# Kernel optimization log

Hardware: AMD Instinct MI355X
Metric: run time of the kernel (lower is better)

The kernel has to match this reference:

```python
import jax, jax.numpy as jnp
import numpy as np

N = 100000  # nodes
E = 1600000  # edges
N_IN, N_H = 256, 128


def _norms(edge_src, edge_dst):
    ones = jnp.ones((E,), dtype=jnp.float32)
    out_deg = jax.ops.segment_sum(ones, edge_src, num_segments=N)
    in_deg = jax.ops.segment_sum(ones, edge_dst, num_segments=N)
    # DGL clamps degrees to >= 1 for norm='both'
    norm_src = jnp.clip(out_deg, 1.0, None) ** -0.5  # [N]
    norm_dst = jnp.clip(in_deg, 1.0, None) ** -0.5   # [N]
    return norm_src, norm_dst


def _graph_conv(h, W, b, edge_src, edge_dst, norm_src, norm_dst):
    # symmetric norm: D_out^{-1/2} A D_in^{-1/2}; W applied pre-aggregation
    h = h * norm_src[:, None]          # [N, d_in]
    h = h @ W                          # [N, d_out]
    msg = h[edge_src]                  # [E, d_out] gather
    agg = jax.ops.segment_sum(msg, edge_dst, num_segments=N)  # scatter-add
    agg = agg * norm_dst[:, None]
    return jax.nn.relu(agg + b)


def setup_inputs() -> dict:
    key = jax.random.key(0)
    ks = jax.random.split(key, 7)
    feat = jax.random.normal(ks[0], (1, N, N_IN), dtype=jnp.float32)
    edge_src = jax.random.randint(ks[1], (E,), 0, N, dtype=jnp.int32)
    edge_dst = jax.random.randint(ks[2], (E,), 0, N, dtype=jnp.int32)
    # Glorot-uniform weights as in DGL GraphConv reset_parameters
    lim1 = (6.0 / (N_IN + N_H)) ** 0.5
    lim2 = (6.0 / (N_H + N_H)) ** 0.5
    W1 = jax.random.uniform(ks[3], (N_IN, N_H), jnp.float32, -lim1, lim1)
    b1 = jnp.zeros((N_H,), dtype=jnp.float32)
    W2 = jax.random.uniform(ks[4], (N_H, N_H), jnp.float32, -lim2, lim2)
    b2 = jnp.zeros((N_H,), dtype=jnp.float32)
    return {"feat": feat, "W1": W1, "b1": b1, "W2": W2, "b2": b2,
            "edge_src": edge_src, "edge_dst": edge_dst}


def reference(feat, W1, b1, W2, b2, edge_src, edge_dst):
    h = feat.squeeze(0)  # [N, n_in]
    norm_src, norm_dst = _norms(edge_src, edge_dst)
    h = _graph_conv(h, W1, b1, edge_src, edge_dst, norm_src, norm_dst)
    h = _graph_conv(h, W2, b2, edge_src, edge_dst, norm_src, norm_dst)
    return h
```

## Files before the change

### kernel.cpp

```cpp
#include <hip/hip_runtime.h>
#include <hip/hip_bf16.h>

#define N_NODES 100000
#define N_EDGES 1600000
#define NBUCK 391
#define NBLK 256
#define CHUNK (N_EDGES / NBLK)
#define MATP (NBUCK * NBLK)

typedef __bf16 bf16x8 __attribute__((ext_vector_type(8)));
typedef float f32x4 __attribute__((ext_vector_type(4)));
typedef unsigned short u16x8 __attribute__((ext_vector_type(8)));
typedef _Float16 f16x8 __attribute__((ext_vector_type(8)));

__device__ __forceinline__ unsigned short f32_to_bf16_rne(float x) {
    unsigned int u = __float_as_uint(x);
    unsigned int r = u + 0x7FFFu + ((u >> 16) & 1u);
    return (unsigned short)(r >> 16);
}
__device__ __forceinline__ float bf16_bits_to_f32(unsigned short h) {
    return __uint_as_float(((unsigned int)h) << 16);
}

__device__ __forceinline__ void wtsplit_elem(const float* __restrict__ W,
                                             unsigned short* __restrict__ WTh,
                                             unsigned short* __restrict__ WTl,
                                             int K, int i) {
    int col = i / K, k = i - col * K;
    float x = W[(size_t)k * 128 + col];
    unsigned short h = f32_to_bf16_rne(x);
    unsigned short l = f32_to_bf16_rne(x - bf16_bits_to_f32(h));
    WTh[i] = h;
    WTl[i] = l;
}

__global__ __launch_bounds__(256) void fused_setup(
    const int* __restrict__ esrc, const int* __restrict__ edst,
    int* __restrict__ cnt_mat,
    const float* __restrict__ W1, unsigned short* __restrict__ WT1h,
    unsigned short* __restrict__ WT1l,
    const float* __restrict__ W2, unsigned short* __restrict__ WT2h,
    unsigned short* __restrict__ WT2l)
{
    __shared__ int hd[NBUCK], hs[NBUCK];
    const int b = blockIdx.x, t = threadIdx.x;
    if (b < NBLK) {
        for (int i = t; i < NBUCK; i += 256) { hd[i] = 0; hs[i] = 0; }
        __syncthreads();
        const int e1 = (b + 1) * CHUNK;
        for (int e = b * CHUNK + t; e < e1; e += 256) {
            atomicAdd(&hd[edst[e] >> 8], 1);
            atomicAdd(&hs[esrc[e] >> 8], 1);
        }
        __syncthreads();
        for (int i = t; i < NBUCK; i += 256) {
            cnt_mat[i * NBLK + b] = hd[i];
            cnt_mat[MATP + i * NBLK + b] = hs[i];
        }
    } else {
        int i = (b - NBLK) * 256 + t;
        if (i < 128 * 256) {
            wtsplit_elem(W1, WT1h, WT1l, 256, i);
        } else {
            int j = i - 128 * 256;
            wtsplit_elem(W2, WT2h, WT2l, 128, j);
        }
    }
}

__global__ __launch_bounds__(1024) void scan_blocks(const int* __restrict__ counts,
                                                    int* __restrict__ out,
                                                    int* __restrict__ partials, int n) {
    __shared__ int tmp[1024];
    int i = blockIdx.x * 1024 + threadIdx.x;
    int v = (i < n) ? counts[i] : 0;
    tmp[threadIdx.x] = v;
    __syncthreads();
    for (int off = 1; off < 1024; off <<= 1) {
        int t = (threadIdx.x >= (unsigned)off) ? tmp[threadIdx.x - off] : 0;
        __syncthreads();
        tmp[threadIdx.x] += t;
        __syncthreads();
    }
    if (i < n) out[i] = tmp[threadIdx.x] - v;
    if (threadIdx.x == 1023) partials[blockIdx.x] = tmp[1023];
}

__global__ void scan_partials(int* __restrict__ partials, int nb) {
    if (threadIdx.x == 0 && blockIdx.x == 0) {
        int s = 0;
        for (int b = 0; b < nb; ++b) { int t = partials[b]; partials[b] = s; s += t; }
    }
}

__device__ __forceinline__ int sm_at(const int* __restrict__ scan_mat,
                                     const int* __restrict__ partials, int i) {
    return scan_mat[i] + partials[i >> 10];
}

__global__ __launch_bounds__(256) void bucket_scatter(const int* __restrict__ esrc,
                                                      const int* __restrict__ edst,
                                                      const int* __restrict__ scan_mat,
                                                      const int* __restrict__ partials,
                                                      unsigned int* __restrict__ tmp) {
    __shared__ int cd[NBUCK], cs[NBUCK];
    const int b = blockIdx.x, t = threadIdx.x;
    for (int i = t; i < NBUCK; i += 256) {
        cd[i] = sm_at(scan_mat, partials, i * NBLK + b);
        cs[i] = sm_at(scan_mat, partials, MATP + i * NBLK + b);
    }
    __syncthreads();
    const int e1 = (b + 1) * CHUNK;
    for (int e = b * CHUNK + t; e < e1; e += 256) {
        int s = esrc[e], d = edst[e];
        int pd = atomicAdd(&cd[d >> 8], 1);
        tmp[pd] = ((unsigned int)(d & 255) << 17) | (unsigned int)s;
        int ps = atomicAdd(&cs[s >> 8], 1);
        tmp[ps] = (unsigned int)s;
    }
}

__global__ __launch_bounds__(256) void finalize_fused(
    const unsigned int* __restrict__ tmp,
    const int* __restrict__ scan_mat,
    const int* __restrict__ partials,
    int* __restrict__ rowptr,
    int* __restrict__ csr_src,
    float* __restrict__ ndst,
    float* __restrict__ nsrc)
{
    __shared__ int hist[256];
    __shared__ int scn[256];
    __shared__ int cur[256];
    const int bb = blockIdx.x, t = threadIdx.x;
    if (bb < NBUCK) {
        const int b = bb;
        const int beg = sm_at(scan_mat, partials, b * 256);
        const int end = sm_at(scan_mat, partials, (b + 1) * 256);
        hist[t] = 0;
        __syncthreads();
        for (int j = beg + t; j < end; j += 256)
            atomicAdd(&hist[tmp[j] >> 17], 1);
        __syncthreads();
        int v = hist[t];
        scn[t] = v;
        __syncthreads();
        for (int off = 1; off < 256; off <<= 1) {
            int u = (t >= off) ? scn[t - off] : 0;
            __syncthreads();
            scn[t] += u;
            __syncthreads();
        }
        int excl = scn[t] - v;
        int node = b * 256 + t;
        if (node <= N_NODES) rowptr[node] = beg + excl;
        if (node < N_NODES) ndst[node] = rsqrtf(fmaxf((float)v, 1.0f));
        cur[t] = beg + excl;
        __syncthreads();
        for (int j = beg + t; j < end; j += 256) {
            unsigned int x = tmp[j];
            int pos = atomicAdd(&cur[x >> 17], 1);
            csr_src[pos] = (int)(x & 0x1FFFFu);
        }
    } else {
        const int b = bb - NBUCK;
        const int beg = sm_at(scan_mat, partials, MATP + b * 256);
        const int end = (b < NBUCK - 1) ? sm_at(scan_mat, partials, MATP + (b + 1) * 256)
                                        : 2 * N_EDGES;
        hist[t] = 0;
        __syncthreads();
        for (int j = beg + t; j < end; j += 256)
            atomicAdd(&hist[tmp[j] & 255u], 1);
        __syncthreads();
        int node = b * 256 + t;
        if (node < N_NODES) nsrc[node] = rsqrtf(fmaxf((float)hist[t], 1.0f));
    }
}

template<int K, typename AT>
__global__ __launch_bounds__(256) void gemm_mfma(
    const AT* __restrict__ A,
    const unsigned short* __restrict__ WTh,
    const unsigned short* __restrict__ WTl,
    const float* __restrict__ rowscale,
    _Float16* __restrict__ C16,
    int M)
{
    constexpr int ASTR = 520;
    constexpr int BSTR = 1032;
    __shared__ unsigned short Ah[4 * ASTR];
    __shared__ unsigned short Al[4 * ASTR];
    __shared__ unsigned short Bh[4 * BSTR];
    __shared__ unsigned short Bl[4 * BSTR];

    const int tid = threadIdx.x;
    const int bm = blockIdx.x * 64;
    const int lane = tid & 63;
    const int wid = tid >> 6;
    const int wm = wid >> 1;
    const int wn = wid & 1;
    const int lr = lane & 15;
    const int lg = lane >> 4;

    const int st_ar = tid >> 2;
    const int st_s8 = tid & 3;
    const int a_row_g = bm + st_ar;

    f32x4 acc[2][4];
    #pragma unroll
    for (int i = 0; i < 2; ++i)
        #pragma unroll
        for (int j = 0; j < 4; ++j)
            acc[i][j] = (f32x4){0.f, 0.f, 0.f, 0.f};

    float avreg[8];
    u16x8 bvh[2], bvl[2];

    auto load_tile = [&](int k0) {
        if (a_row_g < M) {
            const AT* ap = &A[(size_t)a_row_g * K + k0 + st_s8 * 8];
            if constexpr (sizeof(AT) == 4) {
                float4 v0 = *reinterpret_cast<const float4*>(ap);
                float4 v1 = *reinterpret_cast<const float4*>(ap + 4);
                avreg[0] = v0.x; avreg[1] = v0.y; avreg[2] = v0.z; avreg[3] = v0.w;
                avreg[4] = v1.x; avreg[5] = v1.y; avreg[6] = v1.z; avreg[7] = v1.w;
            } else {
                f16x8 v = *reinterpret_cast<const f16x8*>(ap);
                #pragma unroll
                for (int j = 0; j < 8; ++j) avreg[j] = (float)v[j];
            }
        } else {
            #pragma unroll
            for (int j = 0; j < 8; ++j) avreg[j] = 0.f;
        }
        #pragma unroll
        for (int i = 0; i < 2; ++i) {
            int lin = tid + i * 256;
            int col = lin >> 2;
            int s8  = lin & 3;
            const size_t g = (size_t)col * K + k0 + s8 * 8;
            bvh[i] = *reinterpret_cast<const u16x8*>(&WTh[g]);
            bvl[i] = *reinterpret_cast<const u16x8*>(&WTl[g]);
        }
    };

    load_tile(0);

    for (int k0 = 0; k0 < K; k0 += 32) {
        {
            u16x8 vh, vl;
            #pragma unroll
            for (int j = 0; j < 8; ++j) {
                unsigned short h = f32_to_bf16_rne(avreg[j]);
                vh[j] = h;
                vl[j] = f32_to_bf16_rne(avreg[j] - bf16_bits_to_f32(h));
            }
            int off = st_s8 * ASTR + st_ar * 8;
            *reinterpret_cast<u16x8*>(&Ah[off]) = vh;
            *reinterpret_cast<u16x8*>(&Al[off]) = vl;
            #pragma unroll
            for (int i = 0; i < 2; ++i) {
                int lin = tid + i * 256;
                int col = lin >> 2;
                int s8  = lin & 3;
                int boff = s8 * BSTR + col * 8;
                *reinterpret_cast<u16x8*>(&Bh[boff]) = bvh[i];
                *reinterpret_cast<u16x8*>(&Bl[boff]) = bvl[i];
            }
        }
        __syncthreads();

        if (k0 + 32 < K) load_tile(k0 + 32);

        {
            bf16x8 afh[2], afl[2], bfh[4], bfl[4];
            #pragma unroll
            for (int mt = 0; mt < 2; ++mt) {
                int row = wm * 32 + mt * 16 + lr;
                int off = lg * ASTR + row * 8;
                afh[mt] = *reinterpret_cast<const bf16x8*>(&Ah[off]);
                afl[mt] = *reinterpret_cast<const bf16x8*>(&Al[off]);
            }
            #pragma unroll
            for (int nt = 0; nt < 4; ++nt) {
                int col = wn * 64 + nt * 16 + lr;
                int off = lg * BSTR + col * 8;
                bfh[nt] = *reinterpret_cast<const bf16x8*>(&Bh[off]);
                bfl[nt] = *reinterpret_cast<const bf16x8*>(&Bl[off]);
            }
            #pragma unroll
            for (int mt = 0; mt < 2; ++mt) {
                #pragma unroll
                for (int nt = 0; nt < 4; ++nt) {
                    acc[mt][nt] = __builtin_amdgcn_mfma_f32_16x16x32_bf16(
                        afh[mt], bfh[nt], acc[mt][nt], 0, 0, 0);
                    acc[mt][nt] = __builtin_amdgcn_mfma_f32_16x16x32_bf16(
                        afh[mt], bfl[nt], acc[mt][nt], 0, 0, 0);
                    acc[mt][nt] = __builtin_amdgcn_mfma_f32_16x16x32_bf16(
                        afl[mt], bfh[nt], acc[mt][nt], 0, 0, 0);
                }
            }
        }
        __syncthreads();
    }

    #pragma unroll
    for (int mt = 0; mt < 2; ++mt) {
        #pragma unroll
        for (int r = 0; r < 4; ++r) {
            int row = bm + wm * 32 + mt * 16 + lg * 4 + r;
            if (row < M) {
                float s = rowscale[row];
                #pragma unroll
                for (int nt = 0; nt < 4; ++nt) {
                    int col = wn * 64 + nt * 16 + lr;
                    C16[(size_t)row * 128 + col] = (_Float16)(acc[mt][nt][r] * s);
                }
            }
        }
    }
}

template<typename OT>
__global__ __launch_bounds__(256) void aggregate_half(
    const _Float16* __restrict__ h16,
    const int* __restrict__ rowptr,
    const int* __restrict__ csr_src,
    const float* __restrict__ ndst,
    const float* __restrict__ bias,
    OT* __restrict__ out, int N, int c_base)
{
    int g = blockIdx.x * blockDim.x + threadIdx.x;
    int node = g >> 3;
    if (node >= N) return;
    int c8 = ((g & 7) * 8) + c_base;
    int beg = rowptr[node];
    int end = rowptr[node + 1];
    float acc[8] = {0.f, 0.f, 0.f, 0.f, 0.f, 0.f, 0.f, 0.f};
    int j = beg;
    for (; j + 3 < end; j += 4) {
        int s0 = csr_src[j];
        int s1 = csr_src[j + 1];
        int s2 = csr_src[j + 2];
        int s3 = csr_src[j + 3];
        f16x8 v0 = *reinterpret_cast<const f16x8*>(&h16[(size_t)s0 * 128 + c8]);
        f16x8 v1 = *reinterpret_cast<const f16x8*>(&h16[(size_t)s1 * 128 + c8]);
        f16x8 v2 = *reinterpret_cast<const f16x8*>(&h16[(size_t)s2 * 128 + c8]);
        f16x8 v3 = *reinterpret_cast<const f16x8*>(&h16[(size_t)s3 * 128 + c8]);
        #pragma unroll
        for (int k = 0; k < 8; ++k)
            acc[k] += ((float)v0[k] + (float)v1[k]) + ((float)v2[k] + (float)v3[k]);
    }
    for (; j < end; ++j) {
        int s0 = csr_src[j];
        f16x8 v0 = *reinterpret_cast<const f16x8*>(&h16[(size_t)s0 * 128 + c8]);
        #pragma unroll
        for (int k = 0; k < 8; ++k) acc[k] += (float)v0[k];
    }
    float sc = ndst[node];
    const float4 b0 = *reinterpret_cast<const float4*>(&bias[c8]);
    const float4 b1 = *reinterpret_cast<const float4*>(&bias[c8 + 4]);
    float r[8];
    r[0] = fmaxf(acc[0] * sc + b0.x, 0.f);
    r[1] = fmaxf(acc[1] * sc + b0.y, 0.f);
    r[2] = fmaxf(acc[2] * sc + b0.z, 0.f);
    r[3] = fmaxf(acc[3] * sc + b0.w, 0.f);
    r[4] = fmaxf(acc[4] * sc + b1.x, 0.f);
    r[5] = fmaxf(acc[5] * sc + b1.y, 0.f);
    r[6] = fmaxf(acc[6] * sc + b1.z, 0.f);
    r[7] = fmaxf(acc[7] * sc + b1.w, 0.f);
    OT* op = &out[(size_t)node * 128 + c8];
    if constexpr (sizeof(OT) == 4) {
        float4 r0 = {r[0], r[1], r[2], r[3]};
        float4 r1 = {r[4], r[5], r[6], r[7]};
        *reinterpret_cast<float4*>(op) = r0;
        *reinterpret_cast<float4*>(op + 4) = r1;
    } else {
        f16x8 rv;
        #pragma unroll
        for (int k = 0; k < 8; ++k) rv[k] = (_Float16)r[k];
        *reinterpret_cast<f16x8*>(op) = rv;
    }
}

extern "C" void kernel_launch(void* const* d_in, const int* in_sizes, int n_in,
                              void* d_out, int out_size, void* d_ws, size_t ws_size,
                              hipStream_t stream) {
    const float* feat = (const float*)d_in[0];
    const float* W1   = (const float*)d_in[1];
    const float* b1   = (const float*)d_in[2];
    const float* W2   = (const float*)d_in[3];
    const float* b2   = (const float*)d_in[4];
    const int* esrc   = (const int*)d_in[5];
    const int* edst   = (const int*)d_in[6];
    float* out = (float*)d_out;

    const int Nn = N_NODES, E = N_EDGES;
    const int SCAN_N = 2 * MATP;
    const int SCAN_NB = (SCAN_N + 1023) / 1024;

    float* hseg   = (float*)d_ws;
    _Float16* h16   = (_Float16*)hseg;
    _Float16* h1out = h16 + (size_t)Nn * 128;
    unsigned short* WT1h = (unsigned short*)(hseg + (size_t)Nn * 128);
    unsigned short* WT1l = WT1h + 128 * 256;
    unsigned short* WT2h = WT1l + 128 * 256;
    unsigned short* WT2l = WT2h + 128 * 128;
    int* csr_src  = (int*)(WT2l + 128 * 128);
    int* rowptr   = csr_src + E;
    unsigned int* tmp = (unsigned int*)(rowptr + 100004);
    int* cnt_mat  = (int*)(tmp + 2 * (size_t)E);
    int* scan_mat = cnt_mat + SCAN_N;
    int* partials = scan_mat + SCAN_N;
    float* nsrc   = (float*)(partials + ((SCAN_NB + 3) & ~3));
    float* ndst   = nsrc + Nn;

    fused_setup<<<NBLK + 192, 256, 0, stream>>>(esrc, edst, cnt_mat,
                                                W1, WT1h, WT1l, W2, WT2h, WT2l);

    scan_blocks<<<SCAN_NB, 1024, 0, stream>>>(cnt_mat, scan_mat, partials, SCAN_N);
    scan_partials<<<1, 64, 0, stream>>>(partials, SCAN_NB);

    bucket_scatter<<<NBLK, 256, 0, stream>>>(esrc, edst, scan_mat, partials, tmp);
    finalize_fused<<<2 * NBUCK, 256, 0, stream>>>(tmp, scan_mat, partials,
                                                  rowptr, csr_src, ndst, nsrc);

    const int gemm_grid = (Nn + 63) / 64;
    const int aggh_grid = (Nn * 8 + 255) / 256;

    gemm_mfma<256, float><<<gemm_grid, 256, 0, stream>>>(feat, WT1h, WT1l, nsrc, h16, Nn);
    aggregate_half<_Float16><<<aggh_grid, 256, 0, stream>>>(h16, rowptr, csr_src, ndst, b1, h1out, Nn, 0);
    aggregate_half<_Float16><<<aggh_grid, 256, 0, stream>>>(h16, rowptr, csr_src, ndst, b1, h1out, Nn, 64);

    gemm_mfma<128, _Float16><<<gemm_grid, 256, 0, stream>>>(h1out, WT2h, WT2l, nsrc, h16, Nn);
    aggregate_half<float><<<aggh_grid, 256, 0, stream>>>(h16, rowptr, csr_src, ndst, b2, out, Nn, 0);
    aggregate_half<float><<<aggh_grid, 256, 0, stream>>>(h16, rowptr, csr_src, ndst, b2, out, Nn, 64);
}
```

Measured before the change: 267.1 us.

## Switch GEMMs to fp16 MFMA with fewer split terms and merge aggregation launches

Replaces the three-term bf16 split GEMM with fp16 MFMA. The first layer uses two A terms (hi/lo) against a single fp16 weight, and the second layer uses one term because its input is already fp16. This cuts MFMA count, LDS traffic and weight-split work. The two half-channel aggregation launches per layer are merged into one launch, and the serial partials scan becomes a parallel block scan. Dropping the low-order weight term and the low A term in layer 2 lowers precision.

```diff
diff --git a/kernel.cpp b/kernel.cpp
--- a/kernel.cpp
+++ b/kernel.cpp
@@ -8,39 +8,22 @@
 #define CHUNK (N_EDGES / NBLK)
 #define MATP (NBUCK * NBLK)
 
-typedef __bf16 bf16x8 __attribute__((ext_vector_type(8)));
 typedef float f32x4 __attribute__((ext_vector_type(4)));
 typedef unsigned short u16x8 __attribute__((ext_vector_type(8)));
 typedef _Float16 f16x8 __attribute__((ext_vector_type(8)));
 
-__device__ __forceinline__ unsigned short f32_to_bf16_rne(float x) {
-    unsigned int u = __float_as_uint(x);
-    unsigned int r = u + 0x7FFFu + ((u >> 16) & 1u);
-    return (unsigned short)(r >> 16);
-}
-__device__ __forceinline__ float bf16_bits_to_f32(unsigned short h) {
-    return __uint_as_float(((unsigned int)h) << 16);
-}
-
-__device__ __forceinline__ void wtsplit_elem(const float* __restrict__ W,
-                                             unsigned short* __restrict__ WTh,
-                                             unsigned short* __restrict__ WTl,
-                                             int K, int i) {
+__device__ __forceinline__ void wt_elem(const float* __restrict__ W,
+                                        _Float16* __restrict__ WTf,
+                                        int K, int i) {
     int col = i / K, k = i - col * K;
-    float x = W[(size_t)k * 128 + col];
-    unsigned short h = f32_to_bf16_rne(x);
-    unsigned short l = f32_to_bf16_rne(x - bf16_bits_to_f32(h));
-    WTh[i] = h;
-    WTl[i] = l;
+    WTf[i] = (_Float16)W[(size_t)k * 128 + col];
 }
 
 __global__ __launch_bounds__(256) void fused_setup(
     const int* __restrict__ esrc, const int* __restrict__ edst,
     int* __restrict__ cnt_mat,
-    const float* __restrict__ W1, unsigned short* __restrict__ WT1h,
-    unsigned short* __restrict__ WT1l,
-    const float* __restrict__ W2, unsigned short* __restrict__ WT2h,
-    unsigned short* __restrict__ WT2l)
+    const float* __restrict__ W1, _Float16* __restrict__ WT1f,
+    const float* __restrict__ W2, _Float16* __restrict__ WT2f)
 {
     __shared__ int hd[NBUCK], hs[NBUCK];
     const int b = blockIdx.x, t = threadIdx.x;
@@ -60,10 +43,10 @@
     } else {
         int i = (b - NBLK) * 256 + t;
         if (i < 128 * 256) {
-            wtsplit_elem(W1, WT1h, WT1l, 256, i);
+            wt_elem(W1, WT1f, 256, i);
         } else {
             int j = i - 128 * 256;
-            wtsplit_elem(W2, WT2h, WT2l, 128, j);
+            wt_elem(W2, WT2f, 128, j);
         }
     }
 }
@@ -86,11 +69,19 @@
     if (threadIdx.x == 1023) partials[blockIdx.x] = tmp[1023];
 }
 
-__global__ void scan_partials(int* __restrict__ partials, int nb) {
-    if (threadIdx.x == 0 && blockIdx.x == 0) {
-        int s = 0;
-        for (int b = 0; b < nb; ++b) { int t = partials[b]; partials[b] = s; s += t; }
-    }
+__global__ __launch_bounds__(256) void scan_partials(int* __restrict__ partials, int nb) {
+    __shared__ int tmp[256];
+    int t = threadIdx.x;
+    int v = (t < nb) ? partials[t] : 0;
+    tmp[t] = v;
+    __syncthreads();
+    for (int off = 1; off < 256; off <<= 1) {
+        int u = (t >= off) ? tmp[t - off] : 0;
+        __syncthreads();
+        tmp[t] += u;
+        __syncthreads();
+    }
+    if (t < nb) partials[t] = tmp[t] - v;
 }
 
 __device__ __forceinline__ int sm_at(const int* __restrict__ scan_mat,
@@ -177,21 +168,19 @@
     }
 }
 
-template<int K, typename AT>
+template<int K, int ATERMS, typename AT>
 __global__ __launch_bounds__(256) void gemm_mfma(
     const AT* __restrict__ A,
-    const unsigned short* __restrict__ WTh,
-    const unsigned short* __restrict__ WTl,
+    const _Float16* __restrict__ WTf,
     const float* __restrict__ rowscale,
     _Float16* __restrict__ C16,
     int M)
 {
     constexpr int ASTR = 520;
     constexpr int BSTR = 1032;
-    __shared__ unsigned short Ah[4 * ASTR];
-    __shared__ unsigned short Al[4 * ASTR];
-    __shared__ unsigned short Bh[4 * BSTR];
-    __shared__ unsigned short Bl[4 * BSTR];
+    __shared__ _Float16 Ah[4 * ASTR];
+    __shared__ _Float16 Al[ATERMS == 2 ? 4 * ASTR : 8];
+    __shared__ _Float16 Bf[4 * BSTR];
 
     const int tid = threadIdx.x;
     const int bm = blockIdx.x * 64;
@@ -214,7 +203,8 @@
             acc[i][j] = (f32x4){0.f, 0.f, 0.f, 0.f};
 
     float avreg[8];
-    u16x8 bvh[2], bvl[2];
+    f16x8 areg16;
+    f16x8 bv[2];
 
     auto load_tile = [&](int k0) {
         if (a_row_g < M) {
@@ -225,22 +215,23 @@
                 avreg[0] = v0.x; avreg[1] = v0.y; avreg[2] = v0.z; avreg[3] = v0.w;
                 avreg[4] = v1.x; avreg[5] = v1.y; avreg[6] = v1.z; avreg[7] = v1.w;
             } else {
-                f16x8 v = *reinterpret_cast<const f16x8*>(ap);
+                areg16 = *reinterpret_cast<const f16x8*>(ap);
+            }
+        } else {
+            if constexpr (sizeof(AT) == 4) {
                 #pragma unroll
-                for (int j = 0; j < 8; ++j) avreg[j] = (float)v[j];
-            }
-        } else {
-            #pragma unroll
-            for (int j = 0; j < 8; ++j) avreg[j] = 0.f;
+                for (int j = 0; j < 8; ++j) avreg[j] = 0.f;
+            } else {
+                #pragma unroll
+                for (int j = 0; j < 8; ++j) areg16[j] = (_Float16)0.f;
+            }
         }
         #pragma unroll
         for (int i = 0; i < 2; ++i) {
             int lin = tid + i * 256;
             int col = lin >> 2;
             int s8  = lin & 3;
-            const size_t g = (size_t)col * K + k0 + s8 * 8;
-            bvh[i] = *reinterpret_cast<const u16x8*>(&WTh[g]);
-            bvl[i] = *reinterpret_cast<const u16x8*>(&WTl[g]);
+            bv[i] = *reinterpret_cast<const f16x8*>(&WTf[(size_t)col * K + k0 + s8 * 8]);
         }
     };
 
@@ -248,24 +239,27 @@
 
     for (int k0 = 0; k0 < K; k0 += 32) {
         {
-            u16x8 vh, vl;
-            #pragma unroll
-            for (int j = 0; j < 8; ++j) {
-                unsigned short h = f32_to_bf16_rne(avreg[j]);
-                vh[j] = h;
-                vl[j] = f32_to_bf16_rne(avreg[j] - bf16_bits_to_f32(h));
-            }
             int off = st_s8 * ASTR + st_ar * 8;
-            *reinterpret_cast<u16x8*>(&Ah[off]) = vh;
-            *reinterpret_cast<u16x8*>(&Al[off]) = vl;
+            if constexpr (sizeof(AT) == 4) {
+                f16x8 vh, vl;
+                #pragma unroll
+                for (int j = 0; j < 8; ++j) {
+                    _Float16 h = (_Float16)avreg[j];
+                    vh[j] = h;
+                    vl[j] = (_Float16)(avreg[j] - (float)h);
+                }
+                *reinterpret_cast<f16x8*>(&Ah[off]) = vh;
+                if constexpr (ATERMS == 2)
+                    *reinterpret_cast<f16x8*>(&Al[off]) = vl;
+            } else {
+                *reinterpret_cast<f16x8*>(&Ah[off]) = areg16;
+            }
             #pragma unroll
             for (int i = 0; i < 2; ++i) {
                 int lin = tid + i * 256;
                 int col = lin >> 2;
                 int s8  = lin & 3;
-                int boff = s8 * BSTR + col * 8;
-                *reinterpret_cast<u16x8*>(&Bh[boff]) = bvh[i];
-                *reinterpret_cast<u16x8*>(&Bl[boff]) = bvl[i];
+                *reinterpret_cast<f16x8*>(&Bf[s8 * BSTR + col * 8]) = bv[i];
             }
         }
         __syncthreads();
@@ -273,31 +267,29 @@
         if (k0 + 32 < K) load_tile(k0 + 32);
 
         {
-            bf16x8 afh[2], afl[2], bfh[4], bfl[4];
+            f16x8 afh[2], afl[2], bf[4];
             #pragma unroll
             for (int mt = 0; mt < 2; ++mt) {
                 int row = wm * 32 + mt * 16 + lr;
                 int off = lg * ASTR + row * 8;
-                afh[mt] = *reinterpret_cast<const bf16x8*>(&Ah[off]);
-                afl[mt] = *reinterpret_cast<const bf16x8*>(&Al[off]);
+                afh[mt] = *reinterpret_cast<const f16x8*>(&Ah[off]);
+                if constexpr (ATERMS == 2)
+                    afl[mt] = *reinterpret_cast<const f16x8*>(&Al[off]);
             }
             #pragma unroll
             for (int nt = 0; nt < 4; ++nt) {
                 int col = wn * 64 + nt * 16 + lr;
-                int off = lg * BSTR + col * 8;
-                bfh[nt] = *reinterpret_cast<const bf16x8*>(&Bh[off]);
-                bfl[nt] = *reinterpret_cast<const bf16x8*>(&Bl[off]);
+                bf[nt] = *reinterpret_cast<const f16x8*>(&Bf[lg * BSTR + col * 8]);
             }
             #pragma unroll
             for (int mt = 0; mt < 2; ++mt) {
                 #pragma unroll
                 for (int nt = 0; nt < 4; ++nt) {
-                    acc[mt][nt] = __builtin_amdgcn_mfma_f32_16x16x32_bf16(
-                        afh[mt], bfh[nt], acc[mt][nt], 0, 0, 0);
-                    acc[mt][nt] = __builtin_amdgcn_mfma_f32_16x16x32_bf16(
-                        afh[mt], bfl[nt], acc[mt][nt], 0, 0, 0);
-                    acc[mt][nt] = __builtin_amdgcn_mfma_f32_16x16x32_bf16(
-                        afl[mt], bfh[nt], acc[mt][nt], 0, 0, 0);
+                    acc[mt][nt] = __builtin_amdgcn_mfma_f32_16x16x32_f16(
+                        afh[mt], bf[nt], acc[mt][nt], 0, 0, 0);
+                    if constexpr (ATERMS == 2)
+                        acc[mt][nt] = __builtin_amdgcn_mfma_f32_16x16x32_f16(
+                            afl[mt], bf[nt], acc[mt][nt], 0, 0, 0);
                 }
             }
         }
@@ -322,15 +314,18 @@
 }
 
 template<typename OT>
-__global__ __launch_bounds__(256) void aggregate_half(
+__global__ __launch_bounds__(256) void aggregate_full(
     const _Float16* __restrict__ h16,
     const int* __restrict__ rowptr,
     const int* __restrict__ csr_src,
     const float* __restrict__ ndst,
     const float* __restrict__ bias,
-    OT* __restrict__ out, int N, int c_base)
+    OT* __restrict__ out, int N, int half_blocks)
 {
-    int g = blockIdx.x * blockDim.x + threadIdx.x;
+    int b = blockIdx.x;
+    int c_base = 0;
+    if (b >= half_blocks) { c_base = 64; b -= half_blocks; }
+    int g = b * blockDim.x + threadIdx.x;
     int node = g >> 3;
     if (node >= N) return;
     int c8 = ((g & 7) * 8) + c_base;
@@ -402,11 +397,9 @@
     float* hseg   = (float*)d_ws;
     _Float16* h16   = (_Float16*)hseg;
     _Float16* h1out = h16 + (size_t)Nn * 128;
-    unsigned short* WT1h = (unsigned short*)(hseg + (size_t)Nn * 128);
-    unsigned short* WT1l = WT1h + 128 * 256;
-    unsigned short* WT2h = WT1l + 128 * 256;
-    unsigned short* WT2l = WT2h + 128 * 128;
-    int* csr_src  = (int*)(WT2l + 128 * 128);
+    _Float16* WT1f = (_Float16*)(hseg + (size_t)Nn * 128);
+    _Float16* WT2f = WT1f + 128 * 256;
+    int* csr_src  = (int*)(WT2f + 128 * 128);
     int* rowptr   = csr_src + E;
     unsigned int* tmp = (unsigned int*)(rowptr + 100004);
     int* cnt_mat  = (int*)(tmp + 2 * (size_t)E);
@@ -415,11 +408,10 @@
     float* nsrc   = (float*)(partials + ((SCAN_NB + 3) & ~3));
     float* ndst   = nsrc + Nn;
 
-    fused_setup<<<NBLK + 192, 256, 0, stream>>>(esrc, edst, cnt_mat,
-                                                W1, WT1h, WT1l, W2, WT2h, WT2l);
+    fused_setup<<<NBLK + 192, 256, 0, stream>>>(esrc, edst, cnt_mat, W1, WT1f, W2, WT2f);
 
     scan_blocks<<<SCAN_NB, 1024, 0, stream>>>(cnt_mat, scan_mat, partials, SCAN_N);
-    scan_partials<<<1, 64, 0, stream>>>(partials, SCAN_NB);
+    scan_partials<<<1, 256, 0, stream>>>(partials, SCAN_NB);
 
     bucket_scatter<<<NBLK, 256, 0, stream>>>(esrc, edst, scan_mat, partials, tmp);
     finalize_fused<<<2 * NBUCK, 256, 0, stream>>>(tmp, scan_mat, partials,
@@ -428,11 +420,11 @@
     const int gemm_grid = (Nn + 63) / 64;
     const int aggh_grid = (Nn * 8 + 255) / 256;
 
-    gemm_mfma<256, float><<<gemm_grid, 256, 0, stream>>>(feat, WT1h, WT1l, nsrc, h16, Nn);
-    aggregate_half<_Float16><<<aggh_grid, 256, 0, stream>>>(h16, rowptr, csr_src, ndst, b1, h1out, Nn, 0);
-    aggregate_half<_Float16><<<aggh_grid, 256, 0, stream>>>(h16, rowptr, csr_src, ndst, b1, h1out, Nn, 64);
-
-    gemm_mfma<128, _Float16><<<gemm_grid, 256, 0, stream>>>(h1out, WT2h, WT2l, nsrc, h16, Nn);
-    aggregate_half<float><<<aggh_grid, 256, 0, stream>>>(h16, rowptr, csr_src, ndst, b2, out, Nn, 0);
-    aggregate_half<float><<<aggh_grid, 256, 0, stream>>>(h16, rowptr, csr_src, ndst, b2, out, Nn, 64);
-}
+    gemm_mfma<256, 2, float><<<gemm_grid, 256, 0, stream>>>(feat, WT1f, nsrc, h16, Nn);
+    aggregate_full<_Float16><<<2 * aggh_grid, 256, 0, stream>>>(
+        h16, rowptr, csr_src, ndst, b1, h1out, Nn, aggh_grid);
+
+    gemm_mfma<128, 1, _Float16><<<gemm_grid, 256, 0, stream>>>(h1out, WT2f, nsrc, h16, Nn);
+    aggregate_full<float><<<2 * aggh_grid, 256, 0, stream>>>(
+        h16, rowptr, csr_src, ndst, b2, out, Nn, aggh_grid);
+}
```

Result: faster. 223.7 us (-16.2%).
